# Performance work log

Hardware: AMD Instinct MI355X
Metric: run time of the kernel (lower is better)

The kernel has to match this reference:

```python
import jax, jax.numpy as jnp
import numpy as np

N_NODES = 100000
N_EDGES = 3200000
C = 256
NEG_SLOPE = 0.2


def setup_inputs() -> dict:
    key = jax.random.key(0)
    k1, k2, k3, k4 = jax.random.split(key, 4)
    x = jax.random.normal(k1, (N_NODES, C), dtype=jnp.float32)
    # xavier_uniform on (2C, 1): bound = sqrt(6/(2C+1))
    bound = float(np.sqrt(6.0 / (2 * C + 1)))
    att = jax.random.uniform(k2, (2 * C, 1), dtype=jnp.float32, minval=-bound, maxval=bound)
    row = jax.random.randint(k3, (N_EDGES,), 0, N_NODES, dtype=jnp.int64)
    col = jax.random.randint(k4, (N_EDGES,), 0, N_NODES, dtype=jnp.int64)
    edge_index = jnp.stack([row, col], axis=0)
    return {"x": x, "att": att, "edge_index": edge_index}


def reference(x, att, edge_index):
    # Original: alpha = leaky_relu(cat([x[row], x[col]], -1) @ att)
    # Equivalent split form avoids materializing the [E, 2C] concat:
    # alpha_e = (x @ att[:C])[row] + (x @ att[C:])[col]
    row, col = edge_index[0], edge_index[1]
    n = x.shape[0]
    c = x.shape[1]
    s_src = (x @ att[:c]).squeeze(-1)  # (N,)
    s_dst = (x @ att[c:]).squeeze(-1)  # (N,)
    alpha = jax.nn.leaky_relu(s_src[row] + s_dst[col], negative_slope=NEG_SLOPE)  # (E,)
    # scatter_softmax over edges grouped by destination row id
    m = jax.ops.segment_max(alpha, row, num_segments=n)          # (N,)
    e = jnp.exp(alpha - m[row])                                   # (E,)
    denom = jax.ops.segment_sum(e, row, num_segments=n)          # (N,)
    out = e / denom[row]                                          # (E,)
    # torch code transposes [E,1] -> [1,E] before scatter_softmax; squeeze(-1) is a no-op
    return out[None, :]
```

## Files before the change

### kernel.cpp

```cpp
#include <hip/hip_runtime.h>

#define NN 100000
#define NE 3200000
#define CC 256
#define NEG_SLOPE 0.2f

#define FS_S 80
#define FS_P 3
#define FS_PART 40000
#define FS_ESL (NE / FS_S)
#define BLK 1024

typedef __attribute__((ext_vector_type(8))) _Float16 half8;

__global__ __launch_bounds__(256) void node_scores_kernel(
    const float* __restrict__ x,
    const float* __restrict__ att,
    float* __restrict__ s_src,
    float* __restrict__ s_dst) {
  int t    = blockIdx.x * blockDim.x + threadIdx.x;
  int node = t >> 4;
  int gl   = t & 15;
  if (node >= NN) return;
  const float4* xr = (const float4*)(x + (size_t)node * CC) + gl * 4;
  const float4* a0 = (const float4*)att + gl * 4;
  const float4* a1 = (const float4*)(att + CC) + gl * 4;
  float s0 = 0.f, s1 = 0.f;
#pragma unroll
  for (int j = 0; j < 4; ++j) {
    float4 xv = xr[j];
    float4 av = a0[j];
    float4 bv = a1[j];
    s0 += xv.x * av.x + xv.y * av.y + xv.z * av.z + xv.w * av.w;
    s1 += xv.x * bv.x + xv.y * bv.y + xv.z * bv.z + xv.w * bv.w;
  }
#pragma unroll
  for (int m = 8; m >= 1; m >>= 1) {
    s0 += __shfl_xor(s0, m, 64);
    s1 += __shfl_xor(s1, m, 64);
  }
  if (gl == 0) {
    s_src[node] = s0;
    s_dst[node] = s1;
  }
}

__global__ __launch_bounds__(BLK) void fused_segsum_kernel(
    const int* __restrict__ row,
    const int* __restrict__ col,
    const float* __restrict__ s_src,
    const float* __restrict__ s_dst,
    _Float16* __restrict__ e_out,
    float* __restrict__ partial ) {
  __shared__ float acc[FS_PART];
  int s  = blockIdx.x;
  int p  = blockIdx.y;
  int lo = p * FS_PART;
  for (int i = threadIdx.x; i < FS_PART; i += BLK) acc[i] = 0.0f;
  __syncthreads();
  const int4* row4 = (const int4*)(row + s * FS_ESL);
  const int*  cols = col + s * FS_ESL;
  _Float16* eo = e_out + (size_t)s * FS_ESL;
  const int n8 = FS_ESL / 8;

#define FS_SLOT(r, j)                                      \
  do {                                                     \
    int rr = (r)-lo;                                       \
    if ((unsigned)rr < FS_PART) {                          \
      float a = s_src[(r)] + s_dst[cols[8 * i + (j)]];     \
      a = (a > 0.0f) ? a : NEG_SLOPE * a;                  \
      _Float16 h = (_Float16)__expf(a);                    \
      eo[8 * i + (j)] = h;                                 \
      atomicAdd(&acc[rr], (float)h);                       \
    }                                                      \
  } while (0)

  for (int i = threadIdx.x; i < n8; i += BLK) {
    int4 ra = row4[2 * i], rb = row4[2 * i + 1];
    FS_SLOT(ra.x, 0);
    FS_SLOT(ra.y, 1);
    FS_SLOT(ra.z, 2);
    FS_SLOT(ra.w, 3);
    FS_SLOT(rb.x, 4);
    FS_SLOT(rb.y, 5);
    FS_SLOT(rb.z, 6);
    FS_SLOT(rb.w, 7);
  }
#undef FS_SLOT
  __syncthreads();
  int cnt = NN - lo;
  if (cnt > FS_PART) cnt = FS_PART;
  float* outp = partial + (size_t)s * NN + lo;
  for (int i = threadIdx.x; i < cnt; i += BLK) outp[i] = acc[i];
}

__global__ __launch_bounds__(256) void reduce_kernel(
    const float* __restrict__ partial,
    float* __restrict__ denom) {
  int n4 = blockIdx.x * blockDim.x + threadIdx.x;
  if (n4 >= NN / 4) return;
  float4 sum = make_float4(0.f, 0.f, 0.f, 0.f);
#pragma unroll 8
  for (int s = 0; s < FS_S; ++s) {
    float4 v = ((const float4*)(partial + (size_t)s * NN))[n4];
    sum.x += v.x; sum.y += v.y; sum.z += v.z; sum.w += v.w;
  }
  ((float4*)denom)[n4] = make_float4(1.f / sum.x, 1.f / sum.y, 1.f / sum.z, 1.f / sum.w);
}

__global__ __launch_bounds__(256) void edge_div_kernel(
    const int4* __restrict__ row4,
    const half8* __restrict__ e,
    const float* __restrict__ denom,
    float4* __restrict__ out4) {
  int i = blockIdx.x * blockDim.x + threadIdx.x;
  if (i >= NE / 8) return;
  int4 ra = row4[2 * i], rb = row4[2 * i + 1];
  half8 ev = e[i];
  float4 oa, ob;
  oa.x = (float)ev[0] * denom[ra.x];
  oa.y = (float)ev[1] * denom[ra.y];
  oa.z = (float)ev[2] * denom[ra.z];
  oa.w = (float)ev[3] * denom[ra.w];
  ob.x = (float)ev[4] * denom[rb.x];
  ob.y = (float)ev[5] * denom[rb.y];
  ob.z = (float)ev[6] * denom[rb.z];
  ob.w = (float)ev[7] * denom[rb.w];
  out4[2 * i]     = oa;
  out4[2 * i + 1] = ob;
}

extern "C" void kernel_launch(void* const* d_in, const int* in_sizes, int n_in,
                              void* d_out, int out_size, void* d_ws, size_t ws_size,
                              hipStream_t stream) {
  const float* x   = (const float*)d_in[0];
  const float* att = (const float*)d_in[1];
  const int* ei    = (const int*)d_in[2];
  const int* row   = ei;
  const int* col   = ei + NE;
  const int4* row4 = (const int4*)ei;
  float4* out4     = (float4*)d_out;

  float* s_src    = (float*)d_ws;
  float* s_dst    = s_src + NN;
  float* denom    = s_dst + NN;
  _Float16* e_buf = (_Float16*)(denom + NN);
  float* partial  = (float*)(e_buf + NE);

  node_scores_kernel<<<(NN * 16 + 255) / 256, 256, 0, stream>>>(x, att, s_src, s_dst);
  dim3 fs_grid(FS_S, FS_P);
  fused_segsum_kernel<<<fs_grid, BLK, 0, stream>>>(
      row, col, s_src, s_dst, e_buf, partial);
  reduce_kernel<<<(NN / 4 + 255) / 256, 256, 0, stream>>>(partial, denom);
  edge_div_kernel<<<(NE / 8 + 255) / 256, 256, 0, stream>>>(
      row4, (const half8*)e_buf, denom, out4);
}
```

Baseline: 231.8 us.

## Merge four kernels into one cooperative kernel with grid syncs

Replaces the four separate launches (node scores, fused exp and segment sum, partial reduction, edge normalization) with a single cooperative persistent kernel of 240 blocks of 1024 threads, separated by grid-wide syncs. The aim is to remove per-launch overhead and the gaps between kernels. In exchange, the node-score, reduce and divide phases now run with far fewer threads in grid-stride loops, and each phase pays for a grid barrier. The 40000-float shared-memory array applies to every phase, which limits occupancy to one block per CU throughout.

```diff
diff --git a/kernel.cpp b/kernel.cpp
--- a/kernel.cpp
+++ b/kernel.cpp
@@ -1,4 +1,7 @@
 #include <hip/hip_runtime.h>
+#include <hip/hip_cooperative_groups.h>
+
+namespace cg = cooperative_groups;
 
 #define NN 100000
 #define NE 3200000
@@ -9,59 +12,68 @@
 #define FS_P 3
 #define FS_PART 40000
 #define FS_ESL (NE / FS_S)
+#define NBLK 240
 #define BLK 1024
 
 typedef __attribute__((ext_vector_type(8))) _Float16 half8;
 
-__global__ __launch_bounds__(256) void node_scores_kernel(
+__global__ __launch_bounds__(BLK) void mega_kernel(
     const float* __restrict__ x,
     const float* __restrict__ att,
-    float* __restrict__ s_src,
-    float* __restrict__ s_dst) {
-  int t    = blockIdx.x * blockDim.x + threadIdx.x;
-  int node = t >> 4;
-  int gl   = t & 15;
-  if (node >= NN) return;
-  const float4* xr = (const float4*)(x + (size_t)node * CC) + gl * 4;
-  const float4* a0 = (const float4*)att + gl * 4;
-  const float4* a1 = (const float4*)(att + CC) + gl * 4;
-  float s0 = 0.f, s1 = 0.f;
-#pragma unroll
-  for (int j = 0; j < 4; ++j) {
-    float4 xv = xr[j];
-    float4 av = a0[j];
-    float4 bv = a1[j];
-    s0 += xv.x * av.x + xv.y * av.y + xv.z * av.z + xv.w * av.w;
-    s1 += xv.x * bv.x + xv.y * bv.y + xv.z * bv.z + xv.w * bv.w;
-  }
-#pragma unroll
-  for (int m = 8; m >= 1; m >>= 1) {
-    s0 += __shfl_xor(s0, m, 64);
-    s1 += __shfl_xor(s1, m, 64);
-  }
-  if (gl == 0) {
-    s_src[node] = s0;
-    s_dst[node] = s1;
-  }
-}
-
-__global__ __launch_bounds__(BLK) void fused_segsum_kernel(
     const int* __restrict__ row,
     const int* __restrict__ col,
-    const float* __restrict__ s_src,
-    const float* __restrict__ s_dst,
-    _Float16* __restrict__ e_out,
-    float* __restrict__ partial ) {
+    float* __restrict__ s_src,
+    float* __restrict__ s_dst,
+    _Float16* __restrict__ e_buf,
+    float* __restrict__ partial ,
+    float* __restrict__ denom,
+    float4* __restrict__ out4) {
   __shared__ float acc[FS_PART];
-  int s  = blockIdx.x;
-  int p  = blockIdx.y;
-  int lo = p * FS_PART;
-  for (int i = threadIdx.x; i < FS_PART; i += BLK) acc[i] = 0.0f;
-  __syncthreads();
-  const int4* row4 = (const int4*)(row + s * FS_ESL);
-  const int*  cols = col + s * FS_ESL;
-  _Float16* eo = e_out + (size_t)s * FS_ESL;
-  const int n8 = FS_ESL / 8;
+  cg::grid_group grid = cg::this_grid();
+  const int tid = threadIdx.x;
+  const int bid = blockIdx.x;
+
+  {
+    int gl = tid & 15;
+    const float4* a0 = (const float4*)att + gl * 4;
+    const float4* a1 = (const float4*)(att + CC) + gl * 4;
+    float4 av0 = a0[0], av1 = a0[1], av2 = a0[2], av3 = a0[3];
+    float4 bv0 = a1[0], bv1 = a1[1], bv2 = a1[2], bv3 = a1[3];
+    for (int node = bid * (BLK / 16) + (tid >> 4); node < NN;
+         node += NBLK * (BLK / 16)) {
+      const float4* xr = (const float4*)(x + (size_t)node * CC) + gl * 4;
+      float4 x0 = xr[0], x1 = xr[1], x2 = xr[2], x3 = xr[3];
+      float s0 = x0.x * av0.x + x0.y * av0.y + x0.z * av0.z + x0.w * av0.w
+               + x1.x * av1.x + x1.y * av1.y + x1.z * av1.z + x1.w * av1.w
+               + x2.x * av2.x + x2.y * av2.y + x2.z * av2.z + x2.w * av2.w
+               + x3.x * av3.x + x3.y * av3.y + x3.z * av3.z + x3.w * av3.w;
+      float s1 = x0.x * bv0.x + x0.y * bv0.y + x0.z * bv0.z + x0.w * bv0.w
+               + x1.x * bv1.x + x1.y * bv1.y + x1.z * bv1.z + x1.w * bv1.w
+               + x2.x * bv2.x + x2.y * bv2.y + x2.z * bv2.z + x2.w * bv2.w
+               + x3.x * bv3.x + x3.y * bv3.y + x3.z * bv3.z + x3.w * bv3.w;
+#pragma unroll
+      for (int m = 8; m >= 1; m >>= 1) {
+        s0 += __shfl_xor(s0, m, 64);
+        s1 += __shfl_xor(s1, m, 64);
+      }
+      if (gl == 0) {
+        s_src[node] = s0;
+        s_dst[node] = s1;
+      }
+    }
+  }
+  grid.sync();
+
+  {
+    int s  = bid % FS_S;
+    int p  = bid / FS_S;
+    int lo = p * FS_PART;
+    for (int i = tid; i < FS_PART; i += BLK) acc[i] = 0.0f;
+    __syncthreads();
+    const int4* row4 = (const int4*)(row + s * FS_ESL);
+    const int*  cols = col + s * FS_ESL;
+    _Float16* eo = e_buf + (size_t)s * FS_ESL;
+    const int n8 = FS_ESL / 8;
 
 #define FS_SLOT(r, j)                                      \
   do {                                                     \
@@ -75,59 +87,57 @@
     }                                                      \
   } while (0)
 
-  for (int i = threadIdx.x; i < n8; i += BLK) {
-    int4 ra = row4[2 * i], rb = row4[2 * i + 1];
-    FS_SLOT(ra.x, 0);
-    FS_SLOT(ra.y, 1);
-    FS_SLOT(ra.z, 2);
-    FS_SLOT(ra.w, 3);
-    FS_SLOT(rb.x, 4);
-    FS_SLOT(rb.y, 5);
-    FS_SLOT(rb.z, 6);
-    FS_SLOT(rb.w, 7);
+    for (int i = tid; i < n8; i += BLK) {
+      int4 ra = row4[2 * i], rb = row4[2 * i + 1];
+      FS_SLOT(ra.x, 0);
+      FS_SLOT(ra.y, 1);
+      FS_SLOT(ra.z, 2);
+      FS_SLOT(ra.w, 3);
+      FS_SLOT(rb.x, 4);
+      FS_SLOT(rb.y, 5);
+      FS_SLOT(rb.z, 6);
+      FS_SLOT(rb.w, 7);
+    }
+#undef FS_SLOT
+    __syncthreads();
+    int cnt = NN - lo;
+    if (cnt > FS_PART) cnt = FS_PART;
+    float* outp = partial + (size_t)s * NN + lo;
+    for (int i = tid; i < cnt; i += BLK) outp[i] = acc[i];
   }
-#undef FS_SLOT
-  __syncthreads();
-  int cnt = NN - lo;
-  if (cnt > FS_PART) cnt = FS_PART;
-  float* outp = partial + (size_t)s * NN + lo;
-  for (int i = threadIdx.x; i < cnt; i += BLK) outp[i] = acc[i];
-}
+  grid.sync();
 
-__global__ __launch_bounds__(256) void reduce_kernel(
-    const float* __restrict__ partial,
-    float* __restrict__ denom) {
-  int n4 = blockIdx.x * blockDim.x + threadIdx.x;
-  if (n4 >= NN / 4) return;
-  float4 sum = make_float4(0.f, 0.f, 0.f, 0.f);
+  for (int n4 = bid * BLK + tid; n4 < NN / 4; n4 += NBLK * BLK) {
+    float4 sum = make_float4(0.f, 0.f, 0.f, 0.f);
 #pragma unroll 8
-  for (int s = 0; s < FS_S; ++s) {
-    float4 v = ((const float4*)(partial + (size_t)s * NN))[n4];
-    sum.x += v.x; sum.y += v.y; sum.z += v.z; sum.w += v.w;
+    for (int s = 0; s < FS_S; ++s) {
+      float4 v = ((const float4*)(partial + (size_t)s * NN))[n4];
+      sum.x += v.x; sum.y += v.y; sum.z += v.z; sum.w += v.w;
+    }
+    ((float4*)denom)[n4] =
+        make_float4(1.f / sum.x, 1.f / sum.y, 1.f / sum.z, 1.f / sum.w);
   }
-  ((float4*)denom)[n4] = make_float4(1.f / sum.x, 1.f / sum.y, 1.f / sum.z, 1.f / sum.w);
-}
+  grid.sync();
 
-__global__ __launch_bounds__(256) void edge_div_kernel(
-    const int4* __restrict__ row4,
-    const half8* __restrict__ e,
-    const float* __restrict__ denom,
-    float4* __restrict__ out4) {
-  int i = blockIdx.x * blockDim.x + threadIdx.x;
-  if (i >= NE / 8) return;
-  int4 ra = row4[2 * i], rb = row4[2 * i + 1];
-  half8 ev = e[i];
-  float4 oa, ob;
-  oa.x = (float)ev[0] * denom[ra.x];
-  oa.y = (float)ev[1] * denom[ra.y];
-  oa.z = (float)ev[2] * denom[ra.z];
-  oa.w = (float)ev[3] * denom[ra.w];
-  ob.x = (float)ev[4] * denom[rb.x];
-  ob.y = (float)ev[5] * denom[rb.y];
-  ob.z = (float)ev[6] * denom[rb.z];
-  ob.w = (float)ev[7] * denom[rb.w];
-  out4[2 * i]     = oa;
-  out4[2 * i + 1] = ob;
+  {
+    const int4* row4 = (const int4*)row;
+    const half8* e8  = (const half8*)e_buf;
+    for (int i = bid * BLK + tid; i < NE / 8; i += NBLK * BLK) {
+      int4 ra = row4[2 * i], rb = row4[2 * i + 1];
+      half8 ev = e8[i];
+      float4 oa, ob;
+      oa.x = (float)ev[0] * denom[ra.x];
+      oa.y = (float)ev[1] * denom[ra.y];
+      oa.z = (float)ev[2] * denom[ra.z];
+      oa.w = (float)ev[3] * denom[ra.w];
+      ob.x = (float)ev[4] * denom[rb.x];
+      ob.y = (float)ev[5] * denom[rb.y];
+      ob.z = (float)ev[6] * denom[rb.z];
+      ob.w = (float)ev[7] * denom[rb.w];
+      out4[2 * i]     = oa;
+      out4[2 * i + 1] = ob;
+    }
+  }
 }
 
 extern "C" void kernel_launch(void* const* d_in, const int* in_sizes, int n_in,
@@ -138,7 +148,6 @@
   const int* ei    = (const int*)d_in[2];
   const int* row   = ei;
   const int* col   = ei + NE;
-  const int4* row4 = (const int4*)ei;
   float4* out4     = (float4*)d_out;
 
   float* s_src    = (float*)d_ws;
@@ -147,11 +156,10 @@
   _Float16* e_buf = (_Float16*)(denom + NN);
   float* partial  = (float*)(e_buf + NE);
 
-  node_scores_kernel<<<(NN * 16 + 255) / 256, 256, 0, stream>>>(x, att, s_src, s_dst);
-  dim3 fs_grid(FS_S, FS_P);
-  fused_segsum_kernel<<<fs_grid, BLK, 0, stream>>>(
-      row, col, s_src, s_dst, e_buf, partial);
-  reduce_kernel<<<(NN / 4 + 255) / 256, 256, 0, stream>>>(partial, denom);
-  edge_div_kernel<<<(NE / 8 + 255) / 256, 256, 0, stream>>>(
-      row4, (const half8*)e_buf, denom, out4);
+  void* args[] = {(void*)&x,      (void*)&att,    (void*)&row,
+                  (void*)&col,    (void*)&s_src,  (void*)&s_dst,
+                  (void*)&e_buf,  (void*)&partial,(void*)&denom,
+                  (void*)&out4};
+  hipLaunchCooperativeKernel((void*)mega_kernel, dim3(NBLK), dim3(BLK),
+                             args, 0, stream);
 }
```

Result: slower. 344.9 us (+48.8%).

## Recompute edge exponentials in divide pass and store partial sums as bf16

Applied to the files above, without the earlier changes.

The segment-sum kernel no longer writes the per-edge fp16 exponentials. The final divide kernel instead re-reads col indices, gathers s_src and s_dst, and recomputes leaky_relu and exp. The per-slice partial denominators are stored as bf16 rather than fp32, which halves traffic in the write and reduce stages. This trades one E-sized write/read for an extra col read and two gathers, and bf16 partials lose precision in the denominators.

```diff
diff --git a/kernel.cpp b/kernel.cpp
--- a/kernel.cpp
+++ b/kernel.cpp
@@ -11,7 +11,17 @@
 #define FS_ESL (NE / FS_S)
 #define BLK 1024
 
-typedef __attribute__((ext_vector_type(8))) _Float16 half8;
+typedef __attribute__((ext_vector_type(8))) unsigned short ushort8;
+
+__device__ __forceinline__ unsigned short f32_to_bf16(float f) {
+  union { float f; unsigned int u; } v; v.f = f;
+  unsigned int b = v.u + 0x7FFFu + ((v.u >> 16) & 1u);
+  return (unsigned short)(b >> 16);
+}
+__device__ __forceinline__ float bf16_to_f32(unsigned short h) {
+  union { unsigned int u; float f; } v; v.u = ((unsigned int)h) << 16;
+  return v.f;
+}
 
 __global__ __launch_bounds__(256) void node_scores_kernel(
     const float* __restrict__ x,
@@ -50,8 +60,7 @@
     const int* __restrict__ col,
     const float* __restrict__ s_src,
     const float* __restrict__ s_dst,
-    _Float16* __restrict__ e_out,
-    float* __restrict__ partial ) {
+    unsigned short* __restrict__ partial ) {
   __shared__ float acc[FS_PART];
   int s  = blockIdx.x;
   int p  = blockIdx.y;
@@ -60,7 +69,6 @@
   __syncthreads();
   const int4* row4 = (const int4*)(row + s * FS_ESL);
   const int*  cols = col + s * FS_ESL;
-  _Float16* eo = e_out + (size_t)s * FS_ESL;
   const int n8 = FS_ESL / 8;
 
 #define FS_SLOT(r, j)                                      \
@@ -69,9 +77,7 @@
     if ((unsigned)rr < FS_PART) {                          \
       float a = s_src[(r)] + s_dst[cols[8 * i + (j)]];     \
       a = (a > 0.0f) ? a : NEG_SLOPE * a;                  \
-      _Float16 h = (_Float16)__expf(a);                    \
-      eo[8 * i + (j)] = h;                                 \
-      atomicAdd(&acc[rr], (float)h);                       \
+      atomicAdd(&acc[rr], __expf(a));                      \
     }                                                      \
   } while (0)
 
@@ -90,42 +96,64 @@
   __syncthreads();
   int cnt = NN - lo;
   if (cnt > FS_PART) cnt = FS_PART;
-  float* outp = partial + (size_t)s * NN + lo;
-  for (int i = threadIdx.x; i < cnt; i += BLK) outp[i] = acc[i];
+  unsigned short* outp = partial + (size_t)s * NN + lo;
+  for (int i = threadIdx.x; i < cnt; i += BLK) outp[i] = f32_to_bf16(acc[i]);
 }
 
 __global__ __launch_bounds__(256) void reduce_kernel(
-    const float* __restrict__ partial,
+    const unsigned short* __restrict__ partial,
     float* __restrict__ denom) {
-  int n4 = blockIdx.x * blockDim.x + threadIdx.x;
-  if (n4 >= NN / 4) return;
-  float4 sum = make_float4(0.f, 0.f, 0.f, 0.f);
+  int t = blockIdx.x * blockDim.x + threadIdx.x;
+  if (t >= NN / 8) return;
+  float sum[8] = {0.f, 0.f, 0.f, 0.f, 0.f, 0.f, 0.f, 0.f};
 #pragma unroll 8
   for (int s = 0; s < FS_S; ++s) {
-    float4 v = ((const float4*)(partial + (size_t)s * NN))[n4];
-    sum.x += v.x; sum.y += v.y; sum.z += v.z; sum.w += v.w;
+    ushort8 v = ((const ushort8*)(partial + (size_t)s * NN))[t];
+#pragma unroll
+    for (int j = 0; j < 8; ++j) sum[j] += bf16_to_f32(v[j]);
   }
-  ((float4*)denom)[n4] = make_float4(1.f / sum.x, 1.f / sum.y, 1.f / sum.z, 1.f / sum.w);
+  float4 r0 = make_float4(1.f / sum[0], 1.f / sum[1], 1.f / sum[2], 1.f / sum[3]);
+  float4 r1 = make_float4(1.f / sum[4], 1.f / sum[5], 1.f / sum[6], 1.f / sum[7]);
+  ((float4*)denom)[2 * t]     = r0;
+  ((float4*)denom)[2 * t + 1] = r1;
 }
 
 __global__ __launch_bounds__(256) void edge_div_kernel(
     const int4* __restrict__ row4,
-    const half8* __restrict__ e,
+    const int4* __restrict__ col4,
+    const float* __restrict__ s_src,
+    const float* __restrict__ s_dst,
     const float* __restrict__ denom,
     float4* __restrict__ out4) {
   int i = blockIdx.x * blockDim.x + threadIdx.x;
   if (i >= NE / 8) return;
   int4 ra = row4[2 * i], rb = row4[2 * i + 1];
-  half8 ev = e[i];
+  int4 ca = col4[2 * i], cb = col4[2 * i + 1];
+  float a0 = s_src[ra.x] + s_dst[ca.x];
+  float a1 = s_src[ra.y] + s_dst[ca.y];
+  float a2 = s_src[ra.z] + s_dst[ca.z];
+  float a3 = s_src[ra.w] + s_dst[ca.w];
+  float a4 = s_src[rb.x] + s_dst[cb.x];
+  float a5 = s_src[rb.y] + s_dst[cb.y];
+  float a6 = s_src[rb.z] + s_dst[cb.z];
+  float a7 = s_src[rb.w] + s_dst[cb.w];
+  a0 = (a0 > 0.0f) ? a0 : NEG_SLOPE * a0;
+  a1 = (a1 > 0.0f) ? a1 : NEG_SLOPE * a1;
+  a2 = (a2 > 0.0f) ? a2 : NEG_SLOPE * a2;
+  a3 = (a3 > 0.0f) ? a3 : NEG_SLOPE * a3;
+  a4 = (a4 > 0.0f) ? a4 : NEG_SLOPE * a4;
+  a5 = (a5 > 0.0f) ? a5 : NEG_SLOPE * a5;
+  a6 = (a6 > 0.0f) ? a6 : NEG_SLOPE * a6;
+  a7 = (a7 > 0.0f) ? a7 : NEG_SLOPE * a7;
   float4 oa, ob;
-  oa.x = (float)ev[0] * denom[ra.x];
-  oa.y = (float)ev[1] * denom[ra.y];
-  oa.z = (float)ev[2] * denom[ra.z];
-  oa.w = (float)ev[3] * denom[ra.w];
-  ob.x = (float)ev[4] * denom[rb.x];
-  ob.y = (float)ev[5] * denom[rb.y];
-  ob.z = (float)ev[6] * denom[rb.z];
-  ob.w = (float)ev[7] * denom[rb.w];
+  oa.x = __expf(a0) * denom[ra.x];
+  oa.y = __expf(a1) * denom[ra.y];
+  oa.z = __expf(a2) * denom[ra.z];
+  oa.w = __expf(a3) * denom[ra.w];
+  ob.x = __expf(a4) * denom[rb.x];
+  ob.y = __expf(a5) * denom[rb.y];
+  ob.z = __expf(a6) * denom[rb.z];
+  ob.w = __expf(a7) * denom[rb.w];
   out4[2 * i]     = oa;
   out4[2 * i + 1] = ob;
 }
@@ -139,19 +167,18 @@
   const int* row   = ei;
   const int* col   = ei + NE;
   const int4* row4 = (const int4*)ei;
+  const int4* col4 = (const int4*)(ei + NE);
   float4* out4     = (float4*)d_out;
 
-  float* s_src    = (float*)d_ws;
-  float* s_dst    = s_src + NN;
-  float* denom    = s_dst + NN;
-  _Float16* e_buf = (_Float16*)(denom + NN);
-  float* partial  = (float*)(e_buf + NE);
+  float* s_src           = (float*)d_ws;
+  float* s_dst           = s_src + NN;
+  float* denom           = s_dst + NN;
+  unsigned short* partial = (unsigned short*)(denom + NN);
 
   node_scores_kernel<<<(NN * 16 + 255) / 256, 256, 0, stream>>>(x, att, s_src, s_dst);
   dim3 fs_grid(FS_S, FS_P);
-  fused_segsum_kernel<<<fs_grid, BLK, 0, stream>>>(
-      row, col, s_src, s_dst, e_buf, partial);
-  reduce_kernel<<<(NN / 4 + 255) / 256, 256, 0, stream>>>(partial, denom);
+  fused_segsum_kernel<<<fs_grid, BLK, 0, stream>>>(row, col, s_src, s_dst, partial);
+  reduce_kernel<<<(NN / 8 + 255) / 256, 256, 0, stream>>>(partial, denom);
   edge_div_kernel<<<(NE / 8 + 255) / 256, 256, 0, stream>>>(
-      row4, (const half8*)e_buf, denom, out4);
+      row4, col4, s_src, s_dst, denom, out4);
 }
```

Result: slower. 252.6 us (+9.0%).
